# Optimization experiments

Hardware: AMD Instinct MI355X
Metric: run time of the kernel (lower is better)

## Reference

```python
import jax, jax.numpy as jnp
import numpy as np

V = 472      # vocab = 256 + 216
DIM = 472    # must equal V given forward wiring
ED = 944     # d_inner = expand * dim
N = 16       # d_state
K = 4        # d_conv
R = 30       # dt_rank = ceil(dim/16)
DEPTH = 8
B, L = 2, 2048

PNAMES = ['inproj_w','conv_w','conv_b','xproj_w','dt_w','dt_b','Alog','D','outproj_w']

def _block_params(key, stack=None):
    ks = jax.random.split(key, 6)
    shp = lambda s: s if stack is None else (stack,) + s
    nrm = lambda k, s: (jax.random.normal(k, shp(s), jnp.float32) * 0.02)
    Alog = jnp.log(jnp.arange(1, N + 1, dtype=jnp.float32))  # S4D-real init
    Alog = jnp.broadcast_to(Alog, shp((ED, N)))
    return dict(
        inproj_w=nrm(ks[0], (2 * ED, DIM)),
        conv_w=nrm(ks[1], (ED, 1, K)),
        conv_b=jnp.zeros(shp((ED,)), jnp.float32),
        xproj_w=nrm(ks[2], (R + 2 * N, ED)),
        dt_w=nrm(ks[3], (ED, R)),
        dt_b=nrm(ks[4], (ED,)),
        Alog=Alog,
        D=jnp.ones(shp((ED,)), jnp.float32),
        outproj_w=nrm(ks[5], (DIM, ED)))

def mamba_block(x, p):
    # x: (B, L, DIM)
    inproj_w, conv_w, conv_b, xproj_w, dt_w, dt_b, Alog, Dp, outproj_w = p
    xz = x @ inproj_w.T                       # (B, L, 2*ED)
    xi, z = xz[..., :ED], xz[..., ED:]
    # depthwise causal conv1d over time
    xc = jax.lax.conv_general_dilated(
        jnp.swapaxes(xi, 1, 2), conv_w, (1,), [(K - 1, 0)],
        feature_group_count=ED, dimension_numbers=('NCH', 'OIH', 'NCH'))
    xc = jax.nn.silu(xc + conv_b[None, :, None])
    xc = jnp.swapaxes(xc, 1, 2)               # (B, L, ED)
    dbl = xc @ xproj_w.T                      # (B, L, R+2N)
    delta = jax.nn.softplus(dbl[..., :R] @ dt_w.T + dt_b)  # (B, L, ED)
    Bm, C = dbl[..., R:R + N], dbl[..., R + N:]
    A = -jnp.exp(Alog)                        # (ED, N)

    def step(h, inp):
        x_t, d_t, B_t, C_t = inp              # (B,ED),(B,ED),(B,N),(B,N)
        dA = jnp.exp(d_t[:, :, None] * A)     # (B, ED, N)
        h = dA * h + (d_t * x_t)[:, :, None] * B_t[:, None, :]
        return h, jnp.einsum('ben,bn->be', h, C_t)

    h0 = jnp.zeros((x.shape[0], ED, N), x.dtype)
    seq = lambda a: jnp.swapaxes(a, 0, 1)     # (L, B, ...)
    _, ys = jax.lax.scan(step, h0, (seq(xc), seq(delta), seq(Bm), seq(C)))
    y = jnp.swapaxes(ys, 0, 1) + Dp * xc      # (B, L, ED)
    y = y * jax.nn.silu(z)
    return y @ outproj_w.T                    # (B, L, DIM)

block = jax.checkpoint(mamba_block)

def bidir(x, p):
    return block(x, p) + jnp.flip(block(jnp.flip(x, 1), p), 1)

def forward(x, patch_w, patch_b, lm_head_w, p_in, p_lay, p_out):
    # per-token 3x3 patch embedding (valid 3x3 conv on a 3x3 patch == full contraction)
    h = jnp.einsum('blij,vij->blv', x, patch_w[:, 0]) + patch_b   # (B, L, V==DIM)
    h = h + bidir(h, p_in)
    def body(c, p):
        return c + block(c, p), None
    h, _ = jax.lax.scan(body, h, p_lay)
    h = h + bidir(h, p_out)
    return h @ lm_head_w.T                    # (B, L, V)

def setup_inputs() -> dict:
    key = jax.random.key(0)
    ks = jax.random.split(key, 6)
    inp = {'x': jax.random.normal(ks[0], (B, L, 3, 3), jnp.float32)}
    inp['patch_w'] = jax.random.normal(ks[1], (V, 1, 3, 3), jnp.float32) * 0.1
    inp['patch_b'] = jnp.zeros((V,), jnp.float32)
    inp['lm_head_w'] = jax.random.normal(ks[2], (V, DIM), jnp.float32) * 0.02
    for name, kk, st in [('in', ks[3], None), ('lay', ks[4], DEPTH), ('out', ks[5], None)]:
        d = _block_params(kk, st)
        for pn in PNAMES:
            inp[f'{name}_{pn}'] = d[pn]
    return inp

def reference(x, patch_w, patch_b, lm_head_w,
              in_inproj_w, in_conv_w, in_conv_b, in_xproj_w, in_dt_w, in_dt_b, in_Alog, in_D, in_outproj_w,
              lay_inproj_w, lay_conv_w, lay_conv_b, lay_xproj_w, lay_dt_w, lay_dt_b, lay_Alog, lay_D, lay_outproj_w,
              out_inproj_w, out_conv_w, out_conv_b, out_xproj_w, out_dt_w, out_dt_b, out_Alog, out_D, out_outproj_w):
    p_in = (in_inproj_w, in_conv_w, in_conv_b, in_xproj_w, in_dt_w, in_dt_b, in_Alog, in_D, in_outproj_w)
    p_lay = (lay_inproj_w, lay_conv_w, lay_conv_b, lay_xproj_w, lay_dt_w, lay_dt_b, lay_Alog, lay_D, lay_outproj_w)
    p_out = (out_inproj_w, out_conv_w, out_conv_b, out_xproj_w, out_dt_w, out_dt_b, out_Alog, out_D, out_outproj_w)
    return forward(x, patch_w, patch_b, lm_head_w, p_in, p_lay, p_out)
```

## Files before the change

### kernel.cpp

```cpp
#include <hip/hip_runtime.h>
#include <hip/hip_bf16.h>

typedef __hip_bfloat16 bf16;
typedef __attribute__((ext_vector_type(8))) short short8;
typedef __attribute__((ext_vector_type(4))) float v4f;

#define VOC   472
#define DIM   472
#define ED    944
#define ED2   1888
#define NST   16
#define RNK   30
#define NB    2
#define LSEQ  2048
#define BL    4096
#define DEPTH 8
#define CL    16
#define NCH   128

#define DIMP  480
#define EDP   960
#define ED2P  1920
#define VOCP  512
#define DTNP  1024
#define LOG2E 1.44269504088896f

__device__ __forceinline__ float b2f(bf16 v) { return __bfloat162float(v); }
__device__ __forceinline__ bf16  f2b(float v) { return __float2bfloat16(v); }
__device__ __forceinline__ float siluf_(float x) { return x / (1.f + __expf(-x)); }
__device__ __forceinline__ float softplusf_(float x) { return (x > 15.f) ? x : log1pf(__expf(x)); }

__global__ void cvt_w3(const float* __restrict__ s_in, const float* __restrict__ s_lay,
                       const float* __restrict__ s_out, bf16* __restrict__ dst,
                       int N, int K, int NP, int KP)
{
    int d = blockIdx.y;
    const float* src = (d == 0) ? s_in : (d <= 8 ? s_lay + (size_t)(d - 1) * N * K : s_out);
    int idx = blockIdx.x * 256 + threadIdx.x;
    if (idx >= NP * KP) return;
    int n = idx / KP, k = idx - n * KP;
    float v = (n < N && k < K) ? src[(size_t)n * K + k] : 0.f;
    dst[(size_t)d * NP * KP + idx] = f2b(v);
}

__global__ void cvt_w(const float* __restrict__ src, bf16* __restrict__ dst,
                      int N, int K, int NP, int KP)
{
    int idx = blockIdx.x * 256 + threadIdx.x;
    if (idx >= NP * KP) return;
    int n = idx / KP, k = idx - n * KP;
    float v = (n < N && k < K) ? src[(size_t)n * K + k] : 0.f;
    dst[idx] = f2b(v);
}

__global__ void cvt_f32pad3(const float* __restrict__ s_in, const float* __restrict__ s_lay,
                            const float* __restrict__ s_out, float* __restrict__ dst,
                            int N, int NP)
{
    int d = blockIdx.y;
    const float* src = (d == 0) ? s_in : (d <= 8 ? s_lay + (size_t)(d - 1) * N : s_out);
    int idx = blockIdx.x * 256 + threadIdx.x;
    if (idx >= NP) return;
    dst[(size_t)d * NP + idx] = (idx < N) ? src[idx] : 0.f;
}

__global__ void patch_embed(const float* __restrict__ x, const float* __restrict__ pw,
                            const float* __restrict__ pb, float* __restrict__ h,
                            bf16* __restrict__ h16)
{
    int idx = blockIdx.x * 256 + threadIdx.x;
    if (idx >= BL * DIM) return;
    int row = idx / DIM, v = idx - row * DIM;
    float acc = pb[v];
#pragma unroll
    for (int j = 0; j < 9; j++) acc += x[row * 9 + j] * pw[v * 9 + j];
    h[idx] = acc;
    h16[(size_t)row * DIMP + v] = f2b(acc);
}

template<int BM, int BN, int MODE>
__global__ __launch_bounds__(256)
void gemm_t(const bf16* __restrict__ A, int lda,
            const bf16* __restrict__ W, int ldw,
            float* __restrict__ C, bf16* __restrict__ Cb,
            int ldc, int ldcb, int nstore, int K,
            const float* __restrict__ bias)
{
    constexpr int SM = BM / 2, SN = BN / 2, MF = SM / 16, NF = SN / 16;
    constexpr int ABYTES = BM * 64;
    __shared__ __align__(16) char smem[(BM + BN) * 64];
    const int tid = threadIdx.x;
    const int n0 = blockIdx.x * BN, m0 = blockIdx.y * BM;
    const int w = tid >> 6, lane = tid & 63;
    const int wm = w >> 1, wn = w & 1;
    const int lr = lane & 15, q = lane >> 4, q16 = q * 16;
    v4f acc[MF][NF] = {};

    const int rr = tid >> 2, qa = (tid & 3) * 8;
    for (int k0 = 0; k0 < K; k0 += 32) {
#pragma unroll
        for (int u = 0; u < BM / 64; u++)
            __builtin_amdgcn_global_load_lds(
                (const __attribute__((address_space(1))) void*)(A + (size_t)(m0 + rr + u * 64) * lda + qa + k0),
                (__attribute__((address_space(3))) void*)(smem + u * 4096 + tid * 16), 16, 0, 0);
#pragma unroll
        for (int u = 0; u < BN / 64; u++)
            __builtin_amdgcn_global_load_lds(
                (const __attribute__((address_space(1))) void*)(W + (size_t)(n0 + rr + u * 64) * ldw + qa + k0),
                (__attribute__((address_space(3))) void*)(smem + ABYTES + u * 4096 + tid * 16), 16, 0, 0);
        __syncthreads();
        short8 af[MF], bfr[NF];
#pragma unroll
        for (int i = 0; i < MF; i++)
            af[i]  = *(const short8*)(smem + ((wm * SM + i * 16 + lr) * 64 + q16));
#pragma unroll
        for (int j = 0; j < NF; j++)
            bfr[j] = *(const short8*)(smem + ABYTES + ((wn * SN + j * 16 + lr) * 64 + q16));
#pragma unroll
        for (int mi = 0; mi < MF; mi++)
#pragma unroll
            for (int ni = 0; ni < NF; ni++)
                acc[mi][ni] = __builtin_amdgcn_mfma_f32_16x16x32_bf16(af[mi], bfr[ni], acc[mi][ni], 0, 0, 0);
        __syncthreads();
    }
#pragma unroll
    for (int mi = 0; mi < MF; mi++) {
#pragma unroll
        for (int ni = 0; ni < NF; ni++) {
            int col = n0 + wn * SN + ni * 16 + lr;
            if (col < nstore) {
#pragma unroll
                for (int r = 0; r < 4; r++) {
                    int row = m0 + wm * SM + mi * 16 + q * 4 + r;
                    float v = acc[mi][ni][r];
                    if (MODE == 0) C[(size_t)row * ldc + col] = v;
                    else if (MODE == 1) Cb[(size_t)row * ldc + col] = f2b(v);
                    else if (MODE == 2) {
                        float nv = C[(size_t)row * ldc + col] + v;
                        C[(size_t)row * ldc + col] = nv;
                        Cb[(size_t)row * ldcb + col] = f2b(nv);
                    } else {
                        Cb[(size_t)row * ldcb + col] = f2b(softplusf_(v + bias[col]));
                    }
                }
            }
        }
    }
}

__global__ void conv_kernel(const bf16* __restrict__ xz, const float* __restrict__ cw,
                            const float* __restrict__ cb, bf16* __restrict__ xc, int ndir)
{
    int idx = blockIdx.x * 256 + threadIdx.x;
    if (idx >= BL * ED) return;
    int row = idx / ED, e = idx - row * ED;
    int t = row & (LSEQ - 1);
    float w0 = cw[e * 4 + 0], w1 = cw[e * 4 + 1];
    float w2 = cw[e * 4 + 2], w3 = cw[e * 4 + 3];
    float bias = cb[e];
    const bf16* xi = xz + (size_t)row * ED2P + e;
    float acc = bias + w3 * b2f(xi[0]);
    if (t >= 1) acc += w2 * b2f(xi[-1 * ED2P]);
    if (t >= 2) acc += w1 * b2f(xi[-2 * ED2P]);
    if (t >= 3) acc += w0 * b2f(xi[-3 * ED2P]);
    xc[(size_t)row * EDP + e] = f2b(siluf_(acc));
    if (ndir == 2) {
        float a2 = bias + w3 * b2f(xi[0]);
        if (t + 1 < LSEQ) a2 += w2 * b2f(xi[1 * ED2P]);
        if (t + 2 < LSEQ) a2 += w1 * b2f(xi[2 * ED2P]);
        if (t + 3 < LSEQ) a2 += w0 * b2f(xi[3 * ED2P]);
        xc[(size_t)BL * EDP + (size_t)row * EDP + e] = f2b(siluf_(a2));
    }
}


__global__ __launch_bounds__(256)
void scan_passA(const bf16* __restrict__ dblr, const bf16* __restrict__ dlt,
                const bf16* __restrict__ xc, const float* __restrict__ Alog,
                bf16* __restrict__ S, float* __restrict__ sd)
{
    const int e = blockIdx.x * 256 + threadIdx.x;
    const int b = blockIdx.y / NCH;
    const int c = blockIdx.y % NCH;
    const int dir = blockIdx.z;
    __shared__ float Ls[CL][32];
    const bf16* bbase = dblr + ((size_t)dir * BL + b * LSEQ) * 64;
    for (int i = threadIdx.x; i < CL * 32; i += 256) {
        int rowi = i >> 5, j = i & 31;
        int s = c * CL + rowi;
        int t = dir ? (LSEQ - 1 - s) : s;
        Ls[rowi][j] = b2f(bbase[(size_t)t * 64 + 30 + j]);
    }
    __syncthreads();
    if (e >= ED) return;
    const float Av2_0 = -__expf(Alog[e * NST]) * LOG2E;
    const long t0 = dir ? (LSEQ - 1 - c * CL) : (c * CL);
    const long st = dir ? -1 : 1;
    const bf16* dl = dlt + ((size_t)dir * BL + b * LSEQ) * EDP + e;
    const bf16* xp = xc  + ((size_t)dir * BL + b * LSEQ) * EDP + e;
    float dv[CL], xv[CL];
#pragma unroll
    for (int i = 0; i < CL; i++) {
        long off = (t0 + st * i) * EDP;
        dv[i] = b2f(dl[off]);
        xv[i] = b2f(xp[off]);
    }
    float h[NST] = {};
    float sdl = 0.f;
#pragma unroll
    for (int i = 0; i < CL; i++) {
        float delta = dv[i];
        sdl += delta;
        float dx = delta * xv[i];
        float r = exp2f(delta * Av2_0);
        float r2 = r * r;
        float dA0 = r, dA1 = r2, dA2 = r2 * r, dA3 = r2 * r2;
        float r4 = dA3;
#pragma unroll
        for (int g = 0; g < 4; g++) {
            int n = g * 4;
            h[n]     = fmaf(dA0, h[n],     dx * Ls[i][n]);
            h[n + 1] = fmaf(dA1, h[n + 1], dx * Ls[i][n + 1]);
            h[n + 2] = fmaf(dA2, h[n + 2], dx * Ls[i][n + 2]);
            h[n + 3] = fmaf(dA3, h[n + 3], dx * Ls[i][n + 3]);
            if (g < 3) { dA0 *= r4; dA1 *= r4; dA2 *= r4; dA3 *= r4; }
        }
    }
    size_t o = ((((size_t)dir * NB + b) * NCH + c) * ED + e) * NST;
    bf16 hs[NST];
#pragma unroll
    for (int n = 0; n < NST; n++) hs[n] = f2b(h[n]);
    *(short8*)&S[o] = *(const short8*)&hs[0];
    *(short8*)&S[o + 8] = *(const short8*)&hs[8];
    sd[(((size_t)dir * NB + b) * NCH + c) * EDP + e] = sdl;
}

#define PB_CPT 16
#define PB_CGR 8
#define PB_COL 32

__global__ __launch_bounds__(256)
void scan_passB(const bf16* S, const float* __restrict__ sd,
                const float* __restrict__ Alog_in, const float* __restrict__ Alog_lay,
                const float* __restrict__ Alog_out, int lay_idx,
                bf16* Hin)
{
    const int col = threadIdx.x & 31;
    const int cg  = threadIdx.x >> 5;
    const int gcol = blockIdx.x * PB_COL + col;
    const int db = blockIdx.y;
    const int e = gcol >> 4, n = gcol & 15;
    const float* Alog = (lay_idx < 0) ? Alog_in
                       : (lay_idx < DEPTH ? Alog_lay + (size_t)lay_idx * ED * NST : Alog_out);
    const float Av2 = -__expf(Alog[e * NST + n]) * LOG2E;
    const size_t cs  = (size_t)ED * NST;
    const size_t sb  = (size_t)db * NCH * cs + gcol;
    const size_t sdb = (size_t)db * NCH * EDP + e;

    float Hpart[PB_CPT], Pcum[PB_CPT];
    float hloc = 0.f, pc = 1.f;
#pragma unroll
    for (int k = 0; k < PB_CPT; k++) {
        int c = cg * PB_CPT + k;
        float sv = b2f(S[sb + (size_t)c * cs]);
        float pv = exp2f(sd[sdb + (size_t)c * EDP] * Av2);
        Hpart[k] = hloc;
        Pcum[k] = pc;
        hloc = fmaf(pv, hloc, sv);
        pc *= pv;
    }
    __shared__ float Pt[PB_CGR][PB_COL], St[PB_CGR][PB_COL], Pref[PB_CGR][PB_COL];
    Pt[cg][col] = pc;
    St[cg][col] = hloc;
    __syncthreads();
    if (cg == 0) {
        float hp = 0.f;
#pragma unroll
        for (int g = 0; g < PB_CGR; g++) {
            Pref[g][col] = hp;
            hp = fmaf(Pt[g][col], hp, St[g][col]);
        }
    }
    __syncthreads();
    const float hp = Pref[cg][col];
#pragma unroll
    for (int k = 0; k < PB_CPT; k++) {
        int c = cg * PB_CPT + k;
        Hin[sb + (size_t)c * cs] = f2b(fmaf(Pcum[k], hp, Hpart[k]));
    }
}

template<int GATE>
__global__ __launch_bounds__(256)
void scan_passC(const bf16* __restrict__ dblr, const bf16* __restrict__ dlt,
                bf16* __restrict__ xc, const float* __restrict__ Alog,
                const float* __restrict__ Dp, const bf16* __restrict__ Hin,
                const bf16* __restrict__ xz)
{
    const int e = blockIdx.x * 256 + threadIdx.x;
    const int b = blockIdx.y / NCH;
    const int c = blockIdx.y % NCH;
    const int dir = blockIdx.z;
    __shared__ float Ls[CL][32];
    const bf16* bbase = dblr + ((size_t)dir * BL + b * LSEQ) * 64;
    for (int i = threadIdx.x; i < CL * 32; i += 256) {
        int rowi = i >> 5, j = i & 31;
        int s = c * CL + rowi;
        int t = dir ? (LSEQ - 1 - s) : s;
        Ls[rowi][j] = b2f(bbase[(size_t)t * 64 + 30 + j]);
    }
    __syncthreads();
    if (e >= ED) return;
    const float Av2_0 = -__expf(Alog[e * NST]) * LOG2E;
    const long t0 = dir ? (LSEQ - 1 - c * CL) : (c * CL);
    const long st = dir ? -1 : 1;
    const bf16* dl = dlt + ((size_t)dir * BL + b * LSEQ) * EDP + e;
    bf16* xp = xc + ((size_t)dir * BL + b * LSEQ) * EDP + e;
    const bf16* zp = xz + ((size_t)b * LSEQ) * ED2P + ED + e;
    float dv[CL], xv[CL], zv[CL];
#pragma unroll
    for (int i = 0; i < CL; i++) {
        long off = (t0 + st * i) * EDP;
        dv[i] = b2f(dl[off]);
        xv[i] = b2f(xp[off]);
        if (GATE) zv[i] = b2f(zp[(t0 + st * i) * ED2P]);
    }
    size_t o = ((((size_t)dir * NB + b) * NCH + c) * ED + e) * NST;
    bf16 hs[NST];
    *(short8*)&hs[0] = *(const short8*)&Hin[o];
    *(short8*)&hs[8] = *(const short8*)&Hin[o + 8];
    float h[NST];
#pragma unroll
    for (int n = 0; n < NST; n++) h[n] = b2f(hs[n]);
    float Dv = Dp[e];
#pragma unroll
    for (int i = 0; i < CL; i++) {
        float delta = dv[i];
        float dx = delta * xv[i];
        float r = exp2f(delta * Av2_0);
        float r2 = r * r;
        float dA0 = r, dA1 = r2, dA2 = r2 * r, dA3 = r2 * r2;
        float r4 = dA3;
        float y = 0.f;
#pragma unroll
        for (int g = 0; g < 4; g++) {
            int n = g * 4;
            h[n]     = fmaf(dA0, h[n],     dx * Ls[i][n]);
            h[n + 1] = fmaf(dA1, h[n + 1], dx * Ls[i][n + 1]);
            h[n + 2] = fmaf(dA2, h[n + 2], dx * Ls[i][n + 2]);
            h[n + 3] = fmaf(dA3, h[n + 3], dx * Ls[i][n + 3]);
            y = fmaf(h[n],     Ls[i][16 + n],     y);
            y = fmaf(h[n + 1], Ls[i][16 + n + 1], y);
            y = fmaf(h[n + 2], Ls[i][16 + n + 2], y);
            y = fmaf(h[n + 3], Ls[i][16 + n + 3], y);
            if (g < 3) { dA0 *= r4; dA1 *= r4; dA2 *= r4; dA3 *= r4; }
        }
        float yv = y + Dv * xv[i];
        if (GATE) yv *= siluf_(zv[i]);
        xp[(t0 + st * i) * EDP] = f2b(yv);
    }
}

__global__ void silu_mul(bf16* __restrict__ y, const bf16* __restrict__ xz)
{
    int idx = blockIdx.x * 256 + threadIdx.x;
    if (idx >= BL * ED) return;
    int row = idx / ED, e = idx - row * ED;
    float v = b2f(y[(size_t)row * EDP + e]) + b2f(y[(size_t)BL * EDP + (size_t)row * EDP + e]);
    float z = b2f(xz[(size_t)row * ED2P + ED + e]);
    y[(size_t)row * EDP + e] = f2b(v * siluf_(z));
}

struct WS {
    float *hb, *sd, *dtbp;
    bf16 *hb16, *xz16, *xc16, *dblr16, *dlt16, *Sb;
};

static void run_block(const bf16* ip16, const bf16* xp16, const bf16* dt16, const bf16* op16,
                      const float* cw, const float* cb, const float* dtbp_slot,
                      const float* alog, const float* dv,
                      const float* alog_in, const float* alog_lay, const float* alog_out, int lay_idx,
                      int ndir, const WS& ws, hipStream_t stream)
{
    gemm_t<128, 128, 1><<<dim3(ED2P / 128, BL / 128), 256, 0, stream>>>(
        ws.hb16, DIMP, ip16, DIMP, nullptr, ws.xz16, ED2P, 0, ED2P, DIMP, nullptr);
    conv_kernel<<<(BL * ED + 255) / 256, 256, 0, stream>>>(ws.xz16, cw, cb, ws.xc16, ndir);
    gemm_t<64, 64, 1><<<dim3(1, ndir * BL / 64), 256, 0, stream>>>(
        ws.xc16, EDP, xp16, EDP, nullptr, ws.dblr16, 64, 0, 62, EDP, nullptr);
    gemm_t<64, 64, 4><<<dim3(DTNP / 64, ndir * BL / 64), 256, 0, stream>>>(
        ws.dblr16, 64, dt16, 32, nullptr, ws.dlt16, 0, EDP, ED, 32, dtbp_slot);
    scan_passA<<<dim3(4, NB * NCH, ndir), 256, 0, stream>>>(ws.dblr16, ws.dlt16, ws.xc16, alog, ws.Sb, ws.sd);
    scan_passB<<<dim3((ED * NST) / PB_COL, ndir * NB), 256, 0, stream>>>(
        ws.Sb, ws.sd, alog_in, alog_lay, alog_out, lay_idx, ws.Sb);
    if (ndir == 1) {
        scan_passC<1><<<dim3(4, NB * NCH, 1), 256, 0, stream>>>(ws.dblr16, ws.dlt16, ws.xc16, alog, dv, ws.Sb, ws.xz16);
    } else {
        scan_passC<0><<<dim3(4, NB * NCH, 2), 256, 0, stream>>>(ws.dblr16, ws.dlt16, ws.xc16, alog, dv, ws.Sb, ws.xz16);
        silu_mul<<<(BL * ED + 255) / 256, 256, 0, stream>>>(ws.xc16, ws.xz16);
    }
    gemm_t<64, 64, 2><<<dim3(VOCP / 64, BL / 64), 256, 0, stream>>>(
        ws.xc16, EDP, op16, EDP, ws.hb, ws.hb16, DIM, DIMP, DIM, EDP, nullptr);
}

extern "C" void kernel_launch(void* const* d_in, const int* in_sizes, int n_in,
                              void* d_out, int out_size, void* d_ws, size_t ws_size,
                              hipStream_t stream)
{
    (void)in_sizes; (void)n_in; (void)out_size; (void)ws_size;
    const float* x       = (const float*)d_in[0];
    const float* patch_w = (const float*)d_in[1];
    const float* patch_b = (const float*)d_in[2];
    const float* lm_head = (const float*)d_in[3];

    const float* G[3][9];
    for (int g = 0; g < 3; g++)
        for (int i = 0; i < 9; i++) G[g][i] = (const float*)d_in[4 + g * 9 + i];

    char* w = (char*)d_ws;
    auto alloc = [&](size_t bytes) { void* p = w; w += (bytes + 255) & ~(size_t)255; return p; };
    WS ws;
    ws.hb     = (float*)alloc((size_t)BL * DIM * 4);
    ws.hb16   = (bf16*) alloc((size_t)BL * DIMP * 2);
    ws.xz16   = (bf16*) alloc((size_t)BL * ED2P * 2);
    ws.xc16   = (bf16*) alloc((size_t)2 * BL * EDP * 2);
    ws.dblr16 = (bf16*) alloc((size_t)2 * BL * 64 * 2);
    ws.dlt16  = (bf16*) alloc((size_t)2 * BL * EDP * 2);
    ws.Sb     = (bf16*) alloc((size_t)2 * NB * NCH * ED * NST * 2);
    ws.sd     = (float*)alloc((size_t)2 * NB * NCH * EDP * 4);
    ws.dtbp   = (float*)alloc((size_t)10 * EDP * 4);
    const size_t IPSZ = (size_t)ED2P * DIMP;
    const size_t OPSZ = (size_t)VOCP * EDP;
    const size_t DTSZ = (size_t)DTNP * 32;
    const size_t XPSZ = (size_t)64 * EDP;
    bf16* ipw16 = (bf16*)alloc(10 * IPSZ * 2);
    bf16* opw16 = (bf16*)alloc(10 * OPSZ * 2);
    bf16* dtw16 = (bf16*)alloc(10 * DTSZ * 2);
    bf16* xpw16 = (bf16*)alloc(10 * XPSZ * 2);
    bf16* lmw16 = (bf16*)alloc((size_t)VOCP * DIMP * 2);

    cvt_w3<<<dim3((ED2P * DIMP + 255) / 256, 10), 256, 0, stream>>>(
        G[0][0], G[1][0], G[2][0], ipw16, ED2, DIM, ED2P, DIMP);
    cvt_w3<<<dim3((VOCP * EDP + 255) / 256, 10), 256, 0, stream>>>(
        G[0][8], G[1][8], G[2][8], opw16, DIM, ED, VOCP, EDP);
    cvt_w3<<<dim3((DTNP * 32 + 255) / 256, 10), 256, 0, stream>>>(
        G[0][4], G[1][4], G[2][4], dtw16, ED, RNK, DTNP, 32);
    cvt_w3<<<dim3((64 * EDP + 255) / 256, 10), 256, 0, stream>>>(
        G[0][3], G[1][3], G[2][3], xpw16, 62, ED, 64, EDP);
    cvt_w<<<dim3((VOCP * DIMP + 255) / 256), 256, 0, stream>>>(
        lm_head, lmw16, VOC, DIM, VOCP, DIMP);
    cvt_f32pad3<<<dim3((EDP + 255) / 256, 10), 256, 0, stream>>>(
        G[0][5], G[1][5], G[2][5], ws.dtbp, ED, EDP);

    patch_embed<<<(BL * DIM + 255) / 256, 256, 0, stream>>>(x, patch_w, patch_b, ws.hb, ws.hb16);

    run_block(ipw16, xpw16, dtw16, opw16, G[0][1], G[0][2], ws.dtbp, G[0][6], G[0][7],
              G[0][6], G[1][6], G[2][6], -1, 2, ws, stream);

    for (int d = 0; d < DEPTH; d++) {
        run_block(ipw16 + (1 + d) * IPSZ, xpw16 + (1 + d) * XPSZ, dtw16 + (1 + d) * DTSZ,
                  opw16 + (1 + d) * OPSZ,
                  G[1][1] + (size_t)d * ED * 4,
                  G[1][2] + (size_t)d * ED,
                  ws.dtbp + (1 + d) * EDP,
                  G[1][6] + (size_t)d * ED * NST,
                  G[1][7] + (size_t)d * ED,
                  G[0][6], G[1][6], G[2][6], d, 1, ws, stream);
    }

    run_block(ipw16 + 9 * IPSZ, xpw16 + 9 * XPSZ, dtw16 + 9 * DTSZ, opw16 + 9 * OPSZ,
              G[2][1], G[2][2], ws.dtbp + 9 * EDP, G[2][6], G[2][7],
              G[0][6], G[1][6], G[2][6], DEPTH, 2, ws, stream);

    gemm_t<64, 64, 0><<<dim3(VOCP / 64, BL / 64), 256, 0, stream>>>(
        ws.hb16, DIMP, lmw16, DIMP, (float*)d_out, nullptr, VOC, 0, VOC, DIMP, nullptr);
}
```

Measured before the change: 1.505 ms.

## Double-buffer GEMM LDS, vectorize conv/silu_mul, chunk-major delta layout for scan

Three things change. The GEMM now double-buffers its LDS tiles so the next k-slice loads while the current one is computed, and it drops one barrier per iteration. The conv and silu_mul kernels now handle 8 channels per thread with 16-byte loads and stores. The delta GEMM epilogue writes delta in a chunk-major [dir,b,chunk,e,16] layout, so the scan passes can read each 16-step chunk with two vector loads instead of strided scalar loads. The trade-offs are twice the LDS use, which may lower occupancy, and scattered 2-byte stores in the GEMM epilogue.

```diff
diff --git a/kernel.cpp b/kernel.cpp
--- a/kernel.cpp
+++ b/kernel.cpp
@@ -17,6 +17,7 @@
 #define DEPTH 8
 #define CL    16
 #define NCH   128
+#define EDV   118
 
 #define DIMP  480
 #define EDP   960
@@ -27,6 +28,7 @@
 
 __device__ __forceinline__ float b2f(bf16 v) { return __bfloat162float(v); }
 __device__ __forceinline__ bf16  f2b(float v) { return __float2bfloat16(v); }
+__device__ __forceinline__ float sb2f(short s) { return __uint_as_float(((unsigned)(unsigned short)s) << 16); }
 __device__ __forceinline__ float siluf_(float x) { return x / (1.f + __expf(-x)); }
 __device__ __forceinline__ float softplusf_(float x) { return (x > 15.f) ? x : log1pf(__expf(x)); }
 
@@ -88,7 +90,8 @@
 {
     constexpr int SM = BM / 2, SN = BN / 2, MF = SM / 16, NF = SN / 16;
     constexpr int ABYTES = BM * 64;
-    __shared__ __align__(16) char smem[(BM + BN) * 64];
+    constexpr int BUFB = (BM + BN) * 64;
+    __shared__ __align__(16) char smem[2 * BUFB];
     const int tid = threadIdx.x;
     const int n0 = blockIdx.x * BN, m0 = blockIdx.y * BM;
     const int w = tid >> 6, lane = tid & 63;
@@ -97,31 +100,41 @@
     v4f acc[MF][NF] = {};
 
     const int rr = tid >> 2, qa = (tid & 3) * 8;
-    for (int k0 = 0; k0 < K; k0 += 32) {
+    const int NT = K >> 5;
+
+    auto stage = [&](int t, int buf) {
+        const int k0 = t * 32;
+        char* sb = smem + buf * BUFB;
 #pragma unroll
         for (int u = 0; u < BM / 64; u++)
             __builtin_amdgcn_global_load_lds(
                 (const __attribute__((address_space(1))) void*)(A + (size_t)(m0 + rr + u * 64) * lda + qa + k0),
-                (__attribute__((address_space(3))) void*)(smem + u * 4096 + tid * 16), 16, 0, 0);
+                (__attribute__((address_space(3))) void*)(sb + u * 4096 + tid * 16), 16, 0, 0);
 #pragma unroll
         for (int u = 0; u < BN / 64; u++)
             __builtin_amdgcn_global_load_lds(
                 (const __attribute__((address_space(1))) void*)(W + (size_t)(n0 + rr + u * 64) * ldw + qa + k0),
-                (__attribute__((address_space(3))) void*)(smem + ABYTES + u * 4096 + tid * 16), 16, 0, 0);
-        __syncthreads();
+                (__attribute__((address_space(3))) void*)(sb + ABYTES + u * 4096 + tid * 16), 16, 0, 0);
+    };
+
+    stage(0, 0);
+    __syncthreads();
+    for (int t = 0; t < NT; t++) {
+        if (t + 1 < NT) stage(t + 1, (t + 1) & 1);
+        const char* sb = smem + (t & 1) * BUFB;
         short8 af[MF], bfr[NF];
 #pragma unroll
         for (int i = 0; i < MF; i++)
-            af[i]  = *(const short8*)(smem + ((wm * SM + i * 16 + lr) * 64 + q16));
+            af[i]  = *(const short8*)(sb + ((wm * SM + i * 16 + lr) * 64 + q16));
 #pragma unroll
         for (int j = 0; j < NF; j++)
-            bfr[j] = *(const short8*)(smem + ABYTES + ((wn * SN + j * 16 + lr) * 64 + q16));
+            bfr[j] = *(const short8*)(sb + ABYTES + ((wn * SN + j * 16 + lr) * 64 + q16));
 #pragma unroll
         for (int mi = 0; mi < MF; mi++)
 #pragma unroll
             for (int ni = 0; ni < NF; ni++)
                 acc[mi][ni] = __builtin_amdgcn_mfma_f32_16x16x32_bf16(af[mi], bfr[ni], acc[mi][ni], 0, 0, 0);
-        __syncthreads();
+        if (t + 1 < NT) __syncthreads();
     }
 #pragma unroll
     for (int mi = 0; mi < MF; mi++) {
@@ -140,7 +153,10 @@
                         C[(size_t)row * ldc + col] = nv;
                         Cb[(size_t)row * ldcb + col] = f2b(nv);
                     } else {
-                        Cb[(size_t)row * ldcb + col] = f2b(softplusf_(v + bias[col]));
+                        int tt = row & (LSEQ - 1);
+                        int db = row >> 11;
+                        size_t ad = (((size_t)db * NCH + (tt >> 4)) * ED + col) * CL + (tt & 15);
+                        Cb[ad] = f2b(softplusf_(v + bias[col]));
                     }
                 }
             }
@@ -152,24 +168,38 @@
                             const float* __restrict__ cb, bf16* __restrict__ xc, int ndir)
 {
     int idx = blockIdx.x * 256 + threadIdx.x;
-    if (idx >= BL * ED) return;
-    int row = idx / ED, e = idx - row * ED;
+    if (idx >= BL * EDV) return;
+    int row = idx / EDV, g = idx - row * EDV;
+    int e = g * 8;
     int t = row & (LSEQ - 1);
-    float w0 = cw[e * 4 + 0], w1 = cw[e * 4 + 1];
-    float w2 = cw[e * 4 + 2], w3 = cw[e * 4 + 3];
-    float bias = cb[e];
     const bf16* xi = xz + (size_t)row * ED2P + e;
-    float acc = bias + w3 * b2f(xi[0]);
-    if (t >= 1) acc += w2 * b2f(xi[-1 * ED2P]);
-    if (t >= 2) acc += w1 * b2f(xi[-2 * ED2P]);
-    if (t >= 3) acc += w0 * b2f(xi[-3 * ED2P]);
-    xc[(size_t)row * EDP + e] = f2b(siluf_(acc));
+    const short8 zv8 = (short8){0, 0, 0, 0, 0, 0, 0, 0};
+    short8 s0 = *(const short8*)xi;
+    short8 s1 = (t >= 1) ? *(const short8*)(xi - 1 * ED2P) : zv8;
+    short8 s2 = (t >= 2) ? *(const short8*)(xi - 2 * ED2P) : zv8;
+    short8 s3 = (t >= 3) ? *(const short8*)(xi - 3 * ED2P) : zv8;
+    bf16 outF[8];
+#pragma unroll
+    for (int u = 0; u < 8; u++) {
+        float4 wv = *(const float4*)(cw + (size_t)(e + u) * 4);
+        float acc = cb[e + u] + wv.w * sb2f(s0[u]) + wv.z * sb2f(s1[u])
+                  + wv.y * sb2f(s2[u]) + wv.x * sb2f(s3[u]);
+        outF[u] = f2b(siluf_(acc));
+    }
+    *(short8*)(xc + (size_t)row * EDP + e) = *(const short8*)outF;
     if (ndir == 2) {
-        float a2 = bias + w3 * b2f(xi[0]);
-        if (t + 1 < LSEQ) a2 += w2 * b2f(xi[1 * ED2P]);
-        if (t + 2 < LSEQ) a2 += w1 * b2f(xi[2 * ED2P]);
-        if (t + 3 < LSEQ) a2 += w0 * b2f(xi[3 * ED2P]);
-        xc[(size_t)BL * EDP + (size_t)row * EDP + e] = f2b(siluf_(a2));
+        short8 r1 = (t + 1 < LSEQ) ? *(const short8*)(xi + 1 * ED2P) : zv8;
+        short8 r2 = (t + 2 < LSEQ) ? *(const short8*)(xi + 2 * ED2P) : zv8;
+        short8 r3 = (t + 3 < LSEQ) ? *(const short8*)(xi + 3 * ED2P) : zv8;
+        bf16 outR[8];
+#pragma unroll
+        for (int u = 0; u < 8; u++) {
+            float4 wv = *(const float4*)(cw + (size_t)(e + u) * 4);
+            float acc = cb[e + u] + wv.w * sb2f(s0[u]) + wv.z * sb2f(r1[u])
+                      + wv.y * sb2f(r2[u]) + wv.x * sb2f(r3[u]);
+            outR[u] = f2b(siluf_(acc));
+        }
+        *(short8*)(xc + (size_t)BL * EDP + (size_t)row * EDP + e) = *(const short8*)outR;
     }
 }
 
@@ -196,15 +226,23 @@
     const float Av2_0 = -__expf(Alog[e * NST]) * LOG2E;
     const long t0 = dir ? (LSEQ - 1 - c * CL) : (c * CL);
     const long st = dir ? -1 : 1;
-    const bf16* dl = dlt + ((size_t)dir * BL + b * LSEQ) * EDP + e;
-    const bf16* xp = xc  + ((size_t)dir * BL + b * LSEQ) * EDP + e;
+    const int db = dir * NB + b;
+    const int cfw = dir ? (NCH - 1 - c) : c;
+    const bf16* xp = xc + ((size_t)dir * BL + b * LSEQ) * EDP + e;
+    const bf16* dladdr = dlt + (((size_t)db * NCH + cfw) * ED + e) * CL;
+    bf16 darr[CL];
+    *(short8*)&darr[0] = *(const short8*)dladdr;
+    *(short8*)&darr[8] = *(const short8*)(dladdr + 8);
     float dv[CL], xv[CL];
-#pragma unroll
-    for (int i = 0; i < CL; i++) {
-        long off = (t0 + st * i) * EDP;
-        dv[i] = b2f(dl[off]);
-        xv[i] = b2f(xp[off]);
-    }
+    if (dir == 0) {
+#pragma unroll
+        for (int i = 0; i < CL; i++) dv[i] = b2f(darr[i]);
+    } else {
+#pragma unroll
+        for (int i = 0; i < CL; i++) dv[i] = b2f(darr[CL - 1 - i]);
+    }
+#pragma unroll
+    for (int i = 0; i < CL; i++) xv[i] = b2f(xp[(t0 + st * i) * EDP]);
     float h[NST] = {};
     float sdl = 0.f;
 #pragma unroll
@@ -226,13 +264,13 @@
             if (g < 3) { dA0 *= r4; dA1 *= r4; dA2 *= r4; dA3 *= r4; }
         }
     }
-    size_t o = ((((size_t)dir * NB + b) * NCH + c) * ED + e) * NST;
+    size_t o = ((((size_t)db) * NCH + c) * ED + e) * NST;
     bf16 hs[NST];
 #pragma unroll
     for (int n = 0; n < NST; n++) hs[n] = f2b(h[n]);
     *(short8*)&S[o] = *(const short8*)&hs[0];
     *(short8*)&S[o + 8] = *(const short8*)&hs[8];
-    sd[(((size_t)dir * NB + b) * NCH + c) * EDP + e] = sdl;
+    sd[((size_t)db * NCH + c) * EDP + e] = sdl;
 }
 
 #define PB_CPT 16
@@ -314,18 +352,28 @@
     const float Av2_0 = -__expf(Alog[e * NST]) * LOG2E;
     const long t0 = dir ? (LSEQ - 1 - c * CL) : (c * CL);
     const long st = dir ? -1 : 1;
-    const bf16* dl = dlt + ((size_t)dir * BL + b * LSEQ) * EDP + e;
+    const int db = dir * NB + b;
+    const int cfw = dir ? (NCH - 1 - c) : c;
     bf16* xp = xc + ((size_t)dir * BL + b * LSEQ) * EDP + e;
     const bf16* zp = xz + ((size_t)b * LSEQ) * ED2P + ED + e;
+    const bf16* dladdr = dlt + (((size_t)db * NCH + cfw) * ED + e) * CL;
+    bf16 darr[CL];
+    *(short8*)&darr[0] = *(const short8*)dladdr;
+    *(short8*)&darr[8] = *(const short8*)(dladdr + 8);
     float dv[CL], xv[CL], zv[CL];
+    if (dir == 0) {
+#pragma unroll
+        for (int i = 0; i < CL; i++) dv[i] = b2f(darr[i]);
+    } else {
+#pragma unroll
+        for (int i = 0; i < CL; i++) dv[i] = b2f(darr[CL - 1 - i]);
+    }
 #pragma unroll
     for (int i = 0; i < CL; i++) {
-        long off = (t0 + st * i) * EDP;
-        dv[i] = b2f(dl[off]);
-        xv[i] = b2f(xp[off]);
+        xv[i] = b2f(xp[(t0 + st * i) * EDP]);
         if (GATE) zv[i] = b2f(zp[(t0 + st * i) * ED2P]);
     }
-    size_t o = ((((size_t)dir * NB + b) * NCH + c) * ED + e) * NST;
+    size_t o = (((size_t)db * NCH + c) * ED + e) * NST;
     bf16 hs[NST];
     *(short8*)&hs[0] = *(const short8*)&Hin[o];
     *(short8*)&hs[8] = *(const short8*)&Hin[o + 8];
@@ -364,11 +412,19 @@
 __global__ void silu_mul(bf16* __restrict__ y, const bf16* __restrict__ xz)
 {
     int idx = blockIdx.x * 256 + threadIdx.x;
-    if (idx >= BL * ED) return;
-    int row = idx / ED, e = idx - row * ED;
-    float v = b2f(y[(size_t)row * EDP + e]) + b2f(y[(size_t)BL * EDP + (size_t)row * EDP + e]);
-    float z = b2f(xz[(size_t)row * ED2P + ED + e]);
-    y[(size_t)row * EDP + e] = f2b(v * siluf_(z));
+    if (idx >= BL * EDV) return;
+    int row = idx / EDV, g = idx - row * EDV;
+    int e = g * 8;
+    short8 yf = *(const short8*)(y + (size_t)row * EDP + e);
+    short8 yr = *(const short8*)(y + (size_t)BL * EDP + (size_t)row * EDP + e);
+    short8 zz = *(const short8*)(xz + (size_t)row * ED2P + ED + e);
+    bf16 out[8];
+#pragma unroll
+    for (int u = 0; u < 8; u++) {
+        float v = sb2f(yf[u]) + sb2f(yr[u]);
+        out[u] = f2b(v * siluf_(sb2f(zz[u])));
+    }
+    *(short8*)(y + (size_t)row * EDP + e) = *(const short8*)out;
 }
 
 struct WS {
@@ -384,11 +440,11 @@
 {
     gemm_t<128, 128, 1><<<dim3(ED2P / 128, BL / 128), 256, 0, stream>>>(
         ws.hb16, DIMP, ip16, DIMP, nullptr, ws.xz16, ED2P, 0, ED2P, DIMP, nullptr);
-    conv_kernel<<<(BL * ED + 255) / 256, 256, 0, stream>>>(ws.xz16, cw, cb, ws.xc16, ndir);
+    conv_kernel<<<(BL * EDV + 255) / 256, 256, 0, stream>>>(ws.xz16, cw, cb, ws.xc16, ndir);
     gemm_t<64, 64, 1><<<dim3(1, ndir * BL / 64), 256, 0, stream>>>(
         ws.xc16, EDP, xp16, EDP, nullptr, ws.dblr16, 64, 0, 62, EDP, nullptr);
     gemm_t<64, 64, 4><<<dim3(DTNP / 64, ndir * BL / 64), 256, 0, stream>>>(
-        ws.dblr16, 64, dt16, 32, nullptr, ws.dlt16, 0, EDP, ED, 32, dtbp_slot);
+        ws.dblr16, 64, dt16, 32, nullptr, ws.dlt16, 0, 0, ED, 32, dtbp_slot);
     scan_passA<<<dim3(4, NB * NCH, ndir), 256, 0, stream>>>(ws.dblr16, ws.dlt16, ws.xc16, alog, ws.Sb, ws.sd);
     scan_passB<<<dim3((ED * NST) / PB_COL, ndir * NB), 256, 0, stream>>>(
         ws.Sb, ws.sd, alog_in, alog_lay, alog_out, lay_idx, ws.Sb);
@@ -396,7 +452,7 @@
         scan_passC<1><<<dim3(4, NB * NCH, 1), 256, 0, stream>>>(ws.dblr16, ws.dlt16, ws.xc16, alog, dv, ws.Sb, ws.xz16);
     } else {
         scan_passC<0><<<dim3(4, NB * NCH, 2), 256, 0, stream>>>(ws.dblr16, ws.dlt16, ws.xc16, alog, dv, ws.Sb, ws.xz16);
-        silu_mul<<<(BL * ED + 255) / 256, 256, 0, stream>>>(ws.xc16, ws.xz16);
+        silu_mul<<<(BL * EDV + 255) / 256, 256, 0, stream>>>(ws.xc16, ws.xz16);
     }
     gemm_t<64, 64, 2><<<dim3(VOCP / 64, BL / 64), 256, 0, stream>>>(
         ws.xc16, EDP, op16, EDP, ws.hb, ws.hb16, DIM, DIMP, DIM, EDP, nullptr);
@@ -424,7 +480,7 @@
     ws.xz16   = (bf16*) alloc((size_t)BL * ED2P * 2);
     ws.xc16   = (bf16*) alloc((size_t)2 * BL * EDP * 2);
     ws.dblr16 = (bf16*) alloc((size_t)2 * BL * 64 * 2);
-    ws.dlt16  = (bf16*) alloc((size_t)2 * BL * EDP * 2);
+    ws.dlt16  = (bf16*) alloc((size_t)2 * BL * ED * 2);
     ws.Sb     = (bf16*) alloc((size_t)2 * NB * NCH * ED * NST * 2);
     ws.sd     = (float*)alloc((size_t)2 * NB * NCH * EDP * 4);
     ws.dtbp   = (float*)alloc((size_t)10 * EDP * 4);
```

Result: faster. 1.399 ms (-7.1%).
